# Kernel optimization log

Measured on AMD Instinct MI355X. Metric: run time of the kernel, lower is better.

## Reference

```python
import jax, jax.numpy as jnp
import numpy as np
from jax import lax

TWN_THRESHOLD_FACTOR = 0.05
BN_EPS = 1e-5


@jax.custom_vjp
def _ternary_quant(w, t):
    return (w > t).astype(w.dtype) - (w < -t).astype(w.dtype)

def _tq_fwd(w, t):
    mask = (w > t) | (w < -t)
    return _ternary_quant(w, t), mask

def _tq_bwd(mask, g):
    return (g * mask.astype(g.dtype), jnp.zeros((), g.dtype))

_ternary_quant.defvjp(_tq_fwd, _tq_bwd)


def quantize(w):
    # threshold is detached in the original (weight.detach().abs().max())
    t = TWN_THRESHOLD_FACTOR * jnp.max(jnp.abs(lax.stop_gradient(w)))
    return _ternary_quant(w, t)


def conv2d(x, w, b):
    # x: [N,C,H,W], w: [O,I,K,K], valid conv, stride 1
    y = lax.conv_general_dilated(x, w, (1, 1), 'VALID',
                                 dimension_numbers=('NCHW', 'OIHW', 'NCHW'))
    return y + b[None, :, None, None]


def maxpool2(x):
    return lax.reduce_window(x, -jnp.inf, lax.max,
                             (1, 1, 2, 2), (1, 1, 2, 2), 'VALID')


def bn2d(x, g, b):
    # training-mode batch norm over (N,H,W), biased variance
    m = jnp.mean(x, (0, 2, 3), keepdims=True)
    v = jnp.mean(jnp.square(x - m), (0, 2, 3), keepdims=True)
    return (x - m) * lax.rsqrt(v + BN_EPS) * g[None, :, None, None] + b[None, :, None, None]


def bn1d(x, g, b):
    m = jnp.mean(x, 0, keepdims=True)
    v = jnp.mean(jnp.square(x - m), 0, keepdims=True)
    return (x - m) * lax.rsqrt(v + BN_EPS) * g[None, :] + b[None, :]


def setup_inputs() -> dict:
    key = jax.random.key(0)
    ks = jax.random.split(key, 12)
    N = 4096
    inp = {
        'x': jax.random.normal(ks[0], (N, 1, 28, 28), jnp.float32),
        'w1': jax.random.normal(ks[1], (32, 1, 5, 5), jnp.float32) * 0.2,
        'b1': jnp.zeros((32,), jnp.float32),
        'g1': jnp.ones((32,), jnp.float32),
        'be1': jnp.zeros((32,), jnp.float32),
        'w2': jax.random.normal(ks[2], (64, 32, 5, 5), jnp.float32) * 0.05,
        'b2': jnp.zeros((64,), jnp.float32),
        'g2': jnp.ones((64,), jnp.float32),
        'be2': jnp.zeros((64,), jnp.float32),
        'wf1': jax.random.normal(ks[3], (512, 1024), jnp.float32) * 0.03,
        'bf1': jnp.zeros((512,), jnp.float32),
        'g3': jnp.ones((512,), jnp.float32),
        'be3': jnp.zeros((512,), jnp.float32),
        'wf2': jax.random.normal(ks[4], (10, 512), jnp.float32) * 0.04,
        'bf2': jnp.zeros((10,), jnp.float32),
    }
    return inp


def reference(x, w1, b1, g1, be1, w2, b2, g2, be2, wf1, bf1, g3, be3, wf2, bf2):
    h = jax.nn.relu(bn2d(conv2d(x, quantize(w1), b1), g1, be1))     # [N,32,24,24]
    h = maxpool2(h)                                                  # [N,32,12,12]
    h = jax.nn.relu(bn2d(conv2d(h, quantize(w2), b2), g2, be2))     # [N,64,8,8]
    h = maxpool2(h)                                                  # [N,64,4,4]
    h = h.reshape(h.shape[0], -1)                                    # [N,1024]
    h = jax.nn.relu(bn1d(h @ quantize(wf1).T + bf1, g3, be3))       # [N,512]
    return h @ quantize(wf2).T + bf2                                 # [N,10]
```

## Files before the change

kernel.cpp:

```cpp
#include <hip/hip_runtime.h>

#define TID ((int)threadIdx.x)
typedef unsigned short u16;
typedef short short8 __attribute__((ext_vector_type(8)));
typedef float f32x4 __attribute__((ext_vector_type(4)));
typedef float v2f __attribute__((ext_vector_type(2)));

__device__ __forceinline__ u16 f2b(float f) {
    unsigned int x = __float_as_uint(f);
    return (u16)((x + 0x7fffu + ((x >> 16) & 1u)) >> 16);
}
__device__ __forceinline__ float b2f(u16 u) {
    return __uint_as_float(((unsigned int)u) << 16);
}
__device__ __forceinline__ v2f fma2(float a, v2f b, v2f c) {
    v2f av = {a, a};
    return __builtin_elementwise_fma(av, b, c);
}

static constexpr size_t OFF_QW1   = 0;
static constexpr size_t OFF_QWF2  = 3200;
static constexpr size_t OFF_TMAX  = 23680;
static constexpr size_t OFF_SUM1C = 23808;
static constexpr size_t OFF_SSQ1C = 24832;
static constexpr size_t OFF_SUM2  = 25856, OFF_SSQ2 = 26112;
static constexpr size_t OFF_SUM3  = 26368, OFF_SSQ3 = 28416;
static constexpr size_t STATS_BEG = 23680, STATS_END = 30464;
static constexpr size_t OFF_QW2C  = 30720;
static constexpr size_t OFF_QWF1C = 133120;
static constexpr size_t OFF_Y1P   = 1181696;
static constexpr size_t OFF_H2P   = 38930432;
static constexpr size_t OFF_Y3    = 47319040;

__global__ __launch_bounds__(256) void absmax_k(const float* w1, const float* w2,
                                                const float* wf1, const float* wf2,
                                                unsigned int* tmaxbits) {
    int bid = blockIdx.x;
    int b, lb, nb; const float* src; long n;
    if (bid < 1)        { b = 0; src = w1;  n = 800;    lb = bid;       nb = 1;   }
    else if (bid < 9)   { b = 1; src = w2;  n = 51200;  lb = bid - 1;   nb = 8;   }
    else if (bid < 265) { b = 2; src = wf1; n = 524288; lb = bid - 9;   nb = 256; }
    else                { b = 3; src = wf2; n = 5120;   lb = bid - 265; nb = 1;   }
    float m = 0.f;
    for (long i = (long)lb * 256 + TID; i < n; i += (long)nb * 256)
        m = fmaxf(m, fabsf(src[i]));
    __shared__ float red[256];
    red[TID] = m; __syncthreads();
    for (int s = 128; s > 0; s >>= 1) {
        if (TID < s) red[TID] = fmaxf(red[TID], red[TID + s]);
        __syncthreads();
    }
    if (TID == 0) atomicMax(&tmaxbits[b], __float_as_uint(red[0]));
}

__global__ __launch_bounds__(256) void quant_all_k(const float* w1, const float* w2,
                                                   const float* wf1, const float* wf2,
                                                   float* qw1, u16* qw2c, u16* qwf1c,
                                                   float* qwf2, const unsigned int* tmax) {
    int bid = blockIdx.x;
    if (bid < 4) {
        int i = bid * 256 + TID; if (i >= 800) return;
        float t = 0.05f * __uint_as_float(tmax[0]);
        float v = w1[i];
        qw1[i] = (v > t) ? 1.f : ((v < -t) ? -1.f : 0.f);
    } else if (bid < 204) {
        int i = (bid - 4) * 256 + TID;
        float t = 0.05f * __uint_as_float(tmax[1]);
        int ic = i & 31, oc = (i >> 5) & 63, sh = i >> 11;
        float v = w2[(oc * 32 + ic) * 25 + sh];
        qw2c[i] = f2b((v > t) ? 1.f : ((v < -t) ? -1.f : 0.f));
    } else if (bid < 2252) {
        int i = (bid - 204) * 256 + TID;
        float t = 0.05f * __uint_as_float(tmax[2]);
        float v = wf1[i];
        qwf1c[i] = f2b((v > t) ? 1.f : ((v < -t) ? -1.f : 0.f));
    } else {
        int i = (bid - 2252) * 256 + TID;
        float t = 0.05f * __uint_as_float(tmax[3]);
        float v = wf2[i];
        qwf2[i] = (v > t) ? 1.f : ((v < -t) ? -1.f : 0.f);
    }
}

__global__ __launch_bounds__(256) void conv1_fused_k(const float* __restrict__ x,
                                                     const float* __restrict__ qw1,
                                                     u16* __restrict__ y1p,
                                                     float* sum1c, float* ssq1c) {
    __shared__ float wl[800];
    __shared__ float red[4][64];
    for (int i = TID; i < 800; i += 256) wl[i] = qw1[i];
    __syncthreads();
    int p = blockIdx.x * 256 + TID;
    int cg = p & 15, half = (p >> 4) & 1;
    int pr = p >> 5;
    int py = pr % 12, n = pr / 12;
    int l = TID & 63, wv = TID >> 6;
    const float* xb = x + n * 784 + (2 * py) * 28 + half * 12;
    float patch[6][16];
    #pragma unroll
    for (int r = 0; r < 6; r++) {
        const float4* rp = reinterpret_cast<const float4*>(xb + r * 28);
        #pragma unroll
        for (int qq = 0; qq < 4; qq++) {
            float4 v = rp[qq];
            patch[r][qq * 4 + 0] = v.x; patch[r][qq * 4 + 1] = v.y;
            patch[r][qq * 4 + 2] = v.z; patch[r][qq * 4 + 3] = v.w;
        }
    }
    int c0 = cg * 2;
    v2f wp[25];
    #pragma unroll
    for (int k = 0; k < 25; k++)
        wp[k] = (v2f){wl[c0 * 25 + k], wl[(c0 + 1) * 25 + k]};
    v2f A0[12], A1[12];
    #pragma unroll
    for (int ox = 0; ox < 12; ox++) { A0[ox] = (v2f){0.f, 0.f}; A1[ox] = (v2f){0.f, 0.f}; }
    #pragma unroll
    for (int ky = 0; ky < 5; ky++)
        #pragma unroll
        for (int kx = 0; kx < 5; kx++) {
            v2f w = wp[ky * 5 + kx];
            #pragma unroll
            for (int ox = 0; ox < 12; ox++) {
                A0[ox] = fma2(patch[ky][ox + kx], w, A0[ox]);
                A1[ox] = fma2(patch[ky + 1][ox + kx], w, A1[ox]);
            }
        }
    v2f sv = {0.f, 0.f}, qv = {0.f, 0.f};
    #pragma unroll
    for (int ox = 0; ox < 12; ox++) {
        sv += A0[ox] + A1[ox];
        qv = __builtin_elementwise_fma(A0[ox], A0[ox], qv);
        qv = __builtin_elementwise_fma(A1[ox], A1[ox], qv);
    }
    float st[4] = {sv.x, sv.y, qv.x, qv.y};
    u16* base = y1p + (size_t)n * 4608 + (py * 12 + half * 6) * 32 + c0;
    #pragma unroll
    for (int j = 0; j < 6; j++) {
        v2f pm = __builtin_elementwise_max(
                     __builtin_elementwise_max(A0[2 * j], A0[2 * j + 1]),
                     __builtin_elementwise_max(A1[2 * j], A1[2 * j + 1]));
        unsigned int u = (unsigned int)f2b(pm.x) | ((unsigned int)f2b(pm.y) << 16);
        *reinterpret_cast<unsigned int*>(base + j * 32) = u;
    }
    #pragma unroll
    for (int t = 0; t < 4; t++) {
        st[t] += __shfl_xor(st[t], 16);
        st[t] += __shfl_xor(st[t], 32);
    }
    if (l < 16) {
        #pragma unroll
        for (int t = 0; t < 4; t++) red[wv][l * 4 + t] = st[t];
    }
    __syncthreads();
    if (TID < 64) {
        float v = red[0][TID] + red[1][TID] + red[2][TID] + red[3][TID];
        int t = TID & 3, ch = (TID >> 2) * 2 + (t & 1);
        float* dst = (t < 2 ? sum1c : ssq1c) + (blockIdx.x & 7) * 32 + ch;
        atomicAdd(dst, v);
    }
}

__global__ __launch_bounds__(256) void conv2_k(const u16* __restrict__ y1p,
                                               const u16* __restrict__ qw2c,
                                               u16* __restrict__ h2pre,
                                               const float* sum1c, const float* ssq1c,
                                               const float* g1, const float* be1,
                                               float* sum, float* ssq) {
    __shared__ float4 hsm4[1176];
    __shared__ float scs[32], shs[32];
    char* hsraw = (char*)hsm4;
    int n0 = blockIdx.x * 8;
    int l = TID & 63, wv = TID >> 6;
    int oc0 = wv * 16;
    int lm = l & 15, lr = (l >> 3) & 1, ox = l & 7, bq = l >> 4;
    if (TID < 32) {
        float s = 0.f, q = 0.f;
        #pragma unroll
        for (int r = 0; r < 8; r++) { s += sum1c[r * 32 + TID]; q += ssq1c[r * 32 + TID]; }
        float m = s * (1.f / 2359296.f);
        float v = q * (1.f / 2359296.f) - m * m;
        float sc = g1[TID] / sqrtf(v + 1e-5f);
        scs[TID] = sc; shs[TID] = be1[TID] - m * sc;
    }
    __syncthreads();
    float scR[8], shR[8];
    {
        int b = TID & 3;
        #pragma unroll
        for (int j = 0; j < 8; j++) { scR[j] = scs[b * 8 + j]; shR[j] = shs[b * 8 + j]; }
    }
    short8 bw[25];
    #pragma unroll
    for (int sh = 0; sh < 25; sh++)
        bw[sh] = *reinterpret_cast<const short8*>(qw2c + ((size_t)sh * 64 + oc0 + lm) * 32 + bq * 8);
    int xy[5];
    #pragma unroll
    for (int kx = 0; kx < 5; kx++) {
        int xx = ox + kx;
        xy[kx] = lr * 784 + xx * 64 + (((bq + (xx >> 1)) & 3) * 16);
    }
    float sacc = 0.f, s2acc = 0.f;
    {
        const uint4* src = reinterpret_cast<const uint4*>(y1p + (size_t)n0 * 4608);
        #pragma unroll
        for (int k = 0; k < 3; k++) {
            if (k < 2 || TID < 64) {
                int i = TID + k * 256;
                int pix = i >> 2, b = i & 3;
                int y = pix / 12, xx = pix - y * 12;
                union { uint4 v; u16 u[8]; } in, out;
                in.v = src[i];
                #pragma unroll
                for (int j = 0; j < 8; j++)
                    out.u[j] = f2b(fmaxf(fmaf(b2f(in.u[j]), scR[j], shR[j]), 0.f));
                *reinterpret_cast<uint4*>(hsraw + y * 784 + xx * 64 + (((b + (xx >> 1)) & 3) * 16)) = out.v;
            }
        }
    }
    #pragma unroll 1
    for (int s = 0; s < 8; s++) {
        __syncthreads();
        if (s < 7) {
            const uint4* src = reinterpret_cast<const uint4*>(y1p + (size_t)(n0 + s + 1) * 4608);
            char* dst = hsraw + ((s + 1) & 1) * 9408;
            #pragma unroll
            for (int k = 0; k < 3; k++) {
                if (k < 2 || TID < 64) {
                    int i = TID + k * 256;
                    int pix = i >> 2, b = i & 3;
                    int y = pix / 12, xx = pix - y * 12;
                    union { uint4 v; u16 u[8]; } in, out;
                    in.v = src[i];
                    #pragma unroll
                    for (int j = 0; j < 8; j++)
                        out.u[j] = f2b(fmaxf(fmaf(b2f(in.u[j]), scR[j], shR[j]), 0.f));
                    *reinterpret_cast<uint4*>(dst + y * 784 + xx * 64 + (((b + (xx >> 1)) & 3) * 16)) = out.v;
                }
            }
        }
        const char* hb = hsraw + (s & 1) * 9408;
        f32x4 acc[4] = {{0.f,0.f,0.f,0.f},{0.f,0.f,0.f,0.f},{0.f,0.f,0.f,0.f},{0.f,0.f,0.f,0.f}};
        #pragma unroll
        for (int R = 0; R <= 10; R++) {
            short8 a[5];
            #pragma unroll
            for (int kx = 0; kx < 5; kx++)
                a[kx] = *reinterpret_cast<const short8*>(hb + xy[kx] + R * 784);
            #pragma unroll
            for (int mt = 0; mt < 4; mt++) {
                int ky = R - 2 * mt;
                if (ky < 0 || ky > 4) continue;
                #pragma unroll
                for (int kx = 0; kx < 5; kx++)
                    acc[mt] = __builtin_amdgcn_mfma_f32_16x16x32_bf16(a[kx], bw[ky * 5 + kx], acc[mt], 0, 0, 0);
            }
        }
        int n = n0 + s;
        u16* hp = h2pre + (size_t)n * 1024 + (oc0 + lm) * 16;
        #pragma unroll
        for (int mt = 0; mt < 4; mt++) {
            float v0 = acc[mt][0], v1 = acc[mt][1], v2 = acc[mt][2], v3 = acc[mt][3];
            sacc += v0 + v1 + v2 + v3;
            s2acc += v0 * v0 + v1 * v1 + v2 * v2 + v3 * v3;
            float w0 = fmaxf(v0, v1), w1 = fmaxf(v2, v3);
            float p0 = fmaxf(w0, __shfl_xor(w0, 32));
            float p1 = fmaxf(w1, __shfl_xor(w1, 32));
            if (bq < 2) {
                unsigned int u = (unsigned int)f2b(p0) | ((unsigned int)f2b(p1) << 16);
                *reinterpret_cast<unsigned int*>(hp + mt * 4 + bq * 2) = u;
            }
        }
    }
    sacc  += __shfl_xor(sacc, 16);  sacc  += __shfl_xor(sacc, 32);
    s2acc += __shfl_xor(s2acc, 16); s2acc += __shfl_xor(s2acc, 32);
    if (l < 16) { atomicAdd(&sum[oc0 + l], sacc); atomicAdd(&ssq[oc0 + l], s2acc); }
}

__global__ __launch_bounds__(256) void fc1_k(const u16* __restrict__ h2pre,
                                             const u16* __restrict__ qwf1c,
                                             const float* sum2, const float* ssq2,
                                             const float* g2, const float* be2,
                                             float* __restrict__ y3T,
                                             float* sum3, float* ssq3) {
    __shared__ float4 Asm[576], Bsm[576];
    __shared__ float sc2s[64], sh2s[64];
    u16* AsU = (u16*)Asm; u16* BsU = (u16*)Bsm;
    int m0 = blockIdx.x * 64, j0 = blockIdx.y * 64;
    int l = TID & 63, wv = TID >> 6;
    int lm = l & 15, q = l >> 4;
    int r0 = TID >> 3, c0 = TID & 7;
    if (TID < 64) {
        float m = sum2[TID] * (1.f / 262144.f);
        float v = ssq2[TID] * (1.f / 262144.f) - m * m;
        float s = g2[TID] / sqrtf(v + 1e-5f);
        sc2s[TID] = s; sh2s[TID] = be2[TID] - m * s;
    }
    __syncthreads();
    f32x4 acc[4] = {{0.f,0.f,0.f,0.f},{0.f,0.f,0.f,0.f},{0.f,0.f,0.f,0.f},{0.f,0.f,0.f,0.f}};
    #pragma unroll 1
    for (int kc = 0; kc < 16; kc++) {
        int kk = kc * 64;
        if (kc) __syncthreads();
        int oc = (kk + c0 * 8) >> 4;
        float sc = sc2s[oc], sh = sh2s[oc];
        #pragma unroll
        for (int i = 0; i < 2; i++) {
            int r = i * 32 + r0;
            union { float4 v; u16 h[8]; } in, o;
            in.v = *reinterpret_cast<const float4*>(h2pre + (size_t)(m0 + r) * 1024 + kk + c0 * 8);
            #pragma unroll
            for (int e = 0; e < 8; e++)
                o.h[e] = f2b(fmaxf(fmaf(b2f(in.h[e]), sc, sh), 0.f));
            *reinterpret_cast<float4*>(AsU + r * 72 + c0 * 8) = o.v;
            *reinterpret_cast<float4*>(BsU + r * 72 + c0 * 8) =
                *reinterpret_cast<const float4*>(qwf1c + (size_t)(j0 + r) * 1024 + kk + c0 * 8);
        }
        __syncthreads();
        #pragma unroll
        for (int half = 0; half < 2; half++) {
            short8 b = *reinterpret_cast<const short8*>(BsU + (wv * 16 + lm) * 72 + half * 32 + q * 8);
            #pragma unroll
            for (int mt = 0; mt < 4; mt++) {
                short8 a = *reinterpret_cast<const short8*>(AsU + (mt * 16 + lm) * 72 + half * 32 + q * 8);
                acc[mt] = __builtin_amdgcn_mfma_f32_16x16x32_bf16(a, b, acc[mt], 0, 0, 0);
            }
        }
    }
    float s = 0.f, s2 = 0.f;
    #pragma unroll
    for (int mt = 0; mt < 4; mt++) {
        *reinterpret_cast<f32x4*>(y3T + (size_t)(j0 + wv * 16 + lm) * 4096 + m0 + mt * 16 + q * 4) = acc[mt];
        #pragma unroll
        for (int i = 0; i < 4; i++) { float v = acc[mt][i]; s += v; s2 = fmaf(v, v, s2); }
    }
    s  += __shfl_xor(s, 16);  s  += __shfl_xor(s, 32);
    s2 += __shfl_xor(s2, 16); s2 += __shfl_xor(s2, 32);
    if (l < 16) {
        atomicAdd(&sum3[j0 + wv * 16 + l], s);
        atomicAdd(&ssq3[j0 + wv * 16 + l], s2);
    }
}

__global__ __launch_bounds__(256) void fc2_k(const float* __restrict__ y3T,
                                             const float* sum3, const float* ssq3,
                                             const float* g3, const float* be3,
                                             const float* __restrict__ qwf2,
                                             const float* bf2, float* __restrict__ out) {
    __shared__ float wlds[5120];
    __shared__ float part[15][160];
    __shared__ float sc3s[512], sh3s[512];
    for (int i = TID; i < 5120; i += 256) wlds[i] = qwf2[i];
    for (int k = TID; k < 512; k += 256) {
        float m = sum3[k] * (1.f / 4096.f);
        float v = ssq3[k] * (1.f / 4096.f) - m * m;
        float s = g3[k] / sqrtf(v + 1e-5f);
        sc3s[k] = s; sh3s[k] = be3[k] - m * s;
    }
    __syncthreads();
    int nl = TID & 15, ks = TID >> 4;
    int n = blockIdx.x * 16 + nl;
    float acc[10] = {};
    for (int k = ks * 32; k < ks * 32 + 32; k++) {
        float v = fmaxf(y3T[(size_t)k * 4096 + n] * sc3s[k] + sh3s[k], 0.f);
        #pragma unroll
        for (int o = 0; o < 10; o++) acc[o] = fmaf(v, wlds[o * 512 + k], acc[o]);
    }
    if (ks > 0) {
        #pragma unroll
        for (int o = 0; o < 10; o++) part[ks - 1][o * 16 + nl] = acc[o];
    }
    __syncthreads();
    if (ks == 0) {
        #pragma unroll
        for (int o = 0; o < 10; o++) {
            float r = acc[o] + bf2[o];
            #pragma unroll
            for (int j = 0; j < 15; j++) r += part[j][o * 16 + nl];
            out[n * 10 + o] = r;
        }
    }
}

extern "C" void kernel_launch(void* const* d_in, const int* in_sizes, int n_in,
                              void* d_out, int out_size, void* d_ws, size_t ws_size,
                              hipStream_t stream) {
    char* wsb = (char*)d_ws;
    const float* x   = (const float*)d_in[0];
    const float* w1  = (const float*)d_in[1];
    const float* g1  = (const float*)d_in[3];
    const float* be1 = (const float*)d_in[4];
    const float* w2  = (const float*)d_in[5];
    const float* g2  = (const float*)d_in[7];
    const float* be2 = (const float*)d_in[8];
    const float* wf1 = (const float*)d_in[9];
    const float* g3  = (const float*)d_in[11];
    const float* be3 = (const float*)d_in[12];
    const float* wf2 = (const float*)d_in[13];
    const float* bf2 = (const float*)d_in[14];
    float* out = (float*)d_out;

    unsigned int* tmax = (unsigned int*)(wsb + OFF_TMAX);
    float* qw1   = (float*)(wsb + OFF_QW1);
    float* qwf2  = (float*)(wsb + OFF_QWF2);
    u16*   qw2c  = (u16*)(wsb + OFF_QW2C);
    u16*   qwf1c = (u16*)(wsb + OFF_QWF1C);
    u16*   y1p   = (u16*)(wsb + OFF_Y1P);
    u16*   h2pre = (u16*)(wsb + OFF_H2P);
    float* y3    = (float*)(wsb + OFF_Y3);

    float* sum1c = (float*)(wsb + OFF_SUM1C); float* ssq1c = (float*)(wsb + OFF_SSQ1C);
    float* sum2  = (float*)(wsb + OFF_SUM2);  float* ssq2  = (float*)(wsb + OFF_SSQ2);
    float* sum3  = (float*)(wsb + OFF_SUM3);  float* ssq3  = (float*)(wsb + OFF_SSQ3);

    hipMemsetAsync(wsb + STATS_BEG, 0, STATS_END - STATS_BEG, stream);

    absmax_k<<<266, 256, 0, stream>>>(w1, w2, wf1, wf2, tmax);
    quant_all_k<<<2272, 256, 0, stream>>>(w1, w2, wf1, wf2, qw1, qw2c, qwf1c, qwf2, tmax);

    conv1_fused_k<<<6144, 256, 0, stream>>>(x, qw1, y1p, sum1c, ssq1c);
    conv2_k<<<512, 256, 0, stream>>>(y1p, qw2c, h2pre, sum1c, ssq1c, g1, be1, sum2, ssq2);
    fc1_k<<<dim3(64, 8), 256, 0, stream>>>(h2pre, qwf1c, sum2, ssq2, g2, be2, y3, sum3, ssq3);
    fc2_k<<<256, 256, 0, stream>>>(y3, sum3, ssq3, g3, be3, qwf2, bf2, out);
}
```

Before: 232.5 us.

## Fuse fc1 and fc2 into one cooperative kernel with a grid-wide sync

```diff
diff --git a/kernel.cpp b/kernel.cpp
--- a/kernel.cpp
+++ b/kernel.cpp
@@ -1,4 +1,7 @@
 #include <hip/hip_runtime.h>
+#include <hip/hip_cooperative_groups.h>
+
+namespace cg = cooperative_groups;
 
 #define TID ((int)threadIdx.x)
 typedef unsigned short u16;
@@ -30,7 +33,6 @@
 static constexpr size_t OFF_QWF1C = 133120;
 static constexpr size_t OFF_Y1P   = 1181696;
 static constexpr size_t OFF_H2P   = 38930432;
-static constexpr size_t OFF_Y3    = 47319040;
 
 __global__ __launch_bounds__(256) void absmax_k(const float* w1, const float* w2,
                                                 const float* wf1, const float* wf2,
@@ -91,7 +93,7 @@
     for (int i = TID; i < 800; i += 256) wl[i] = qw1[i];
     __syncthreads();
     int p = blockIdx.x * 256 + TID;
-    int cg = p & 15, half = (p >> 4) & 1;
+    int cg_ = p & 15, half = (p >> 4) & 1;
     int pr = p >> 5;
     int py = pr % 12, n = pr / 12;
     int l = TID & 63, wv = TID >> 6;
@@ -107,7 +109,7 @@
             patch[r][qq * 4 + 2] = v.z; patch[r][qq * 4 + 3] = v.w;
         }
     }
-    int c0 = cg * 2;
+    int c0 = cg_ * 2;
     v2f wp[25];
     #pragma unroll
     for (int k = 0; k < 25; k++)
@@ -277,16 +279,24 @@
     if (l < 16) { atomicAdd(&sum[oc0 + l], sacc); atomicAdd(&ssq[oc0 + l], s2acc); }
 }
 
-__global__ __launch_bounds__(256) void fc1_k(const u16* __restrict__ h2pre,
-                                             const u16* __restrict__ qwf1c,
-                                             const float* sum2, const float* ssq2,
-                                             const float* g2, const float* be2,
-                                             float* __restrict__ y3T,
-                                             float* sum3, float* ssq3) {
+__global__ __launch_bounds__(256) void fc12_k(const u16* __restrict__ h2pre,
+                                              const u16* __restrict__ qwf1c,
+                                              const float* sum2, const float* ssq2,
+                                              const float* g2, const float* be2,
+                                              const float* __restrict__ qwf2,
+                                              const float* g3, const float* be3,
+                                              const float* bf2,
+                                              float* sum3, float* ssq3,
+                                              float* __restrict__ out) {
     __shared__ float4 Asm[576], Bsm[576];
     __shared__ float sc2s[64], sh2s[64];
+    __shared__ u16 vls[64 * 74];
+    __shared__ float part[3][640];
+    __shared__ float wsl[640];
     u16* AsU = (u16*)Asm; u16* BsU = (u16*)Bsm;
-    int m0 = blockIdx.x * 64, j0 = blockIdx.y * 64;
+    int bid = blockIdx.x;
+    int jb = bid & 7, mb = bid >> 3;
+    int j0 = jb * 64;
     int l = TID & 63, wv = TID >> 6;
     int lm = l & 15, q = l >> 4;
     int r0 = TID >> 3, c0 = TID & 7;
@@ -296,88 +306,99 @@
         float s = g2[TID] / sqrtf(v + 1e-5f);
         sc2s[TID] = s; sh2s[TID] = be2[TID] - m * s;
     }
+    for (int i = TID; i < 640; i += 256) {
+        int jj = i / 10, o = i - jj * 10;
+        wsl[jj * 10 + o] = qwf2[o * 512 + j0 + jj];
+    }
     __syncthreads();
-    f32x4 acc[4] = {{0.f,0.f,0.f,0.f},{0.f,0.f,0.f,0.f},{0.f,0.f,0.f,0.f},{0.f,0.f,0.f,0.f}};
+    f32x4 acc[2][4] = {};
     #pragma unroll 1
-    for (int kc = 0; kc < 16; kc++) {
-        int kk = kc * 64;
-        if (kc) __syncthreads();
-        int oc = (kk + c0 * 8) >> 4;
-        float sc = sc2s[oc], sh = sh2s[oc];
-        #pragma unroll
-        for (int i = 0; i < 2; i++) {
-            int r = i * 32 + r0;
-            union { float4 v; u16 h[8]; } in, o;
-            in.v = *reinterpret_cast<const float4*>(h2pre + (size_t)(m0 + r) * 1024 + kk + c0 * 8);
-            #pragma unroll
-            for (int e = 0; e < 8; e++)
-                o.h[e] = f2b(fmaxf(fmaf(b2f(in.h[e]), sc, sh), 0.f));
-            *reinterpret_cast<float4*>(AsU + r * 72 + c0 * 8) = o.v;
-            *reinterpret_cast<float4*>(BsU + r * 72 + c0 * 8) =
-                *reinterpret_cast<const float4*>(qwf1c + (size_t)(j0 + r) * 1024 + kk + c0 * 8);
-        }
-        __syncthreads();
-        #pragma unroll
-        for (int half = 0; half < 2; half++) {
-            short8 b = *reinterpret_cast<const short8*>(BsU + (wv * 16 + lm) * 72 + half * 32 + q * 8);
-            #pragma unroll
-            for (int mt = 0; mt < 4; mt++) {
-                short8 a = *reinterpret_cast<const short8*>(AsU + (mt * 16 + lm) * 72 + half * 32 + q * 8);
-                acc[mt] = __builtin_amdgcn_mfma_f32_16x16x32_bf16(a, b, acc[mt], 0, 0, 0);
+    for (int t = 0; t < 2; t++) {
+        int m0 = (mb * 2 + t) * 64;
+        #pragma unroll 1
+        for (int kc = 0; kc < 16; kc++) {
+            int kk = kc * 64;
+            if (kc | t) __syncthreads();
+            int oc = (kk + c0 * 8) >> 4;
+            float sc = sc2s[oc], sh = sh2s[oc];
+            #pragma unroll
+            for (int i = 0; i < 2; i++) {
+                int r = i * 32 + r0;
+                union { float4 v; u16 h[8]; } in, o;
+                in.v = *reinterpret_cast<const float4*>(h2pre + (size_t)(m0 + r) * 1024 + kk + c0 * 8);
+                #pragma unroll
+                for (int e = 0; e < 8; e++)
+                    o.h[e] = f2b(fmaxf(fmaf(b2f(in.h[e]), sc, sh), 0.f));
+                *reinterpret_cast<float4*>(AsU + r * 72 + c0 * 8) = o.v;
+                *reinterpret_cast<float4*>(BsU + r * 72 + c0 * 8) =
+                    *reinterpret_cast<const float4*>(qwf1c + (size_t)(j0 + r) * 1024 + kk + c0 * 8);
+            }
+            __syncthreads();
+            #pragma unroll
+            for (int half = 0; half < 2; half++) {
+                short8 b = *reinterpret_cast<const short8*>(BsU + (wv * 16 + lm) * 72 + half * 32 + q * 8);
+                #pragma unroll
+                for (int mt = 0; mt < 4; mt++) {
+                    short8 a = *reinterpret_cast<const short8*>(AsU + (mt * 16 + lm) * 72 + half * 32 + q * 8);
+                    acc[t][mt] = __builtin_amdgcn_mfma_f32_16x16x32_bf16(a, b, acc[t][mt], 0, 0, 0);
+                }
             }
         }
     }
     float s = 0.f, s2 = 0.f;
     #pragma unroll
-    for (int mt = 0; mt < 4; mt++) {
-        *reinterpret_cast<f32x4*>(y3T + (size_t)(j0 + wv * 16 + lm) * 4096 + m0 + mt * 16 + q * 4) = acc[mt];
-        #pragma unroll
-        for (int i = 0; i < 4; i++) { float v = acc[mt][i]; s += v; s2 = fmaf(v, v, s2); }
-    }
+    for (int t = 0; t < 2; t++)
+        #pragma unroll
+        for (int mt = 0; mt < 4; mt++)
+            #pragma unroll
+            for (int i = 0; i < 4; i++) { float v = acc[t][mt][i]; s += v; s2 = fmaf(v, v, s2); }
     s  += __shfl_xor(s, 16);  s  += __shfl_xor(s, 32);
     s2 += __shfl_xor(s2, 16); s2 += __shfl_xor(s2, 32);
     if (l < 16) {
         atomicAdd(&sum3[j0 + wv * 16 + l], s);
         atomicAdd(&ssq3[j0 + wv * 16 + l], s2);
     }
-}
-
-__global__ __launch_bounds__(256) void fc2_k(const float* __restrict__ y3T,
-                                             const float* sum3, const float* ssq3,
-                                             const float* g3, const float* be3,
-                                             const float* __restrict__ qwf2,
-                                             const float* bf2, float* __restrict__ out) {
-    __shared__ float wlds[5120];
-    __shared__ float part[15][160];
-    __shared__ float sc3s[512], sh3s[512];
-    for (int i = TID; i < 5120; i += 256) wlds[i] = qwf2[i];
-    for (int k = TID; k < 512; k += 256) {
-        float m = sum3[k] * (1.f / 4096.f);
-        float v = ssq3[k] * (1.f / 4096.f) - m * m;
-        float s = g3[k] / sqrtf(v + 1e-5f);
-        sc3s[k] = s; sh3s[k] = be3[k] - m * s;
-    }
-    __syncthreads();
-    int nl = TID & 15, ks = TID >> 4;
-    int n = blockIdx.x * 16 + nl;
-    float acc[10] = {};
-    for (int k = ks * 32; k < ks * 32 + 32; k++) {
-        float v = fmaxf(y3T[(size_t)k * 4096 + n] * sc3s[k] + sh3s[k], 0.f);
-        #pragma unroll
-        for (int o = 0; o < 10; o++) acc[o] = fmaf(v, wlds[o * 512 + k], acc[o]);
-    }
-    if (ks > 0) {
-        #pragma unroll
-        for (int o = 0; o < 10; o++) part[ks - 1][o * 16 + nl] = acc[o];
-    }
-    __syncthreads();
-    if (ks == 0) {
-        #pragma unroll
-        for (int o = 0; o < 10; o++) {
-            float r = acc[o] + bf2[o];
-            #pragma unroll
-            for (int j = 0; j < 15; j++) r += part[j][o * 16 + nl];
-            out[n * 10 + o] = r;
+    __threadfence();
+    cg::this_grid().sync();
+    int j = j0 + wv * 16 + lm;
+    float m3 = sum3[j] * (1.f / 4096.f);
+    float v3 = ssq3[j] * (1.f / 4096.f) - m3 * m3;
+    float sc3 = g3[j] / sqrtf(v3 + 1e-5f);
+    float sh3 = be3[j] - m3 * sc3;
+    int jl = wv * 16 + lm;
+    int ml = TID & 63, grp = TID >> 6;
+    #pragma unroll 1
+    for (int t = 0; t < 2; t++) {
+        int m0 = (mb * 2 + t) * 64;
+        __syncthreads();
+        #pragma unroll
+        for (int mt = 0; mt < 4; mt++)
+            #pragma unroll
+            for (int i = 0; i < 4; i++) {
+                int mrow = mt * 16 + q * 4 + i;
+                vls[mrow * 74 + jl] = f2b(fmaxf(fmaf(acc[t][mt][i], sc3, sh3), 0.f));
+            }
+        __syncthreads();
+        float o10[10] = {};
+        #pragma unroll
+        for (int jj = 0; jj < 16; jj++) {
+            float vj = b2f(vls[ml * 74 + grp * 16 + jj]);
+            #pragma unroll
+            for (int o = 0; o < 10; o++)
+                o10[o] = fmaf(vj, wsl[(grp * 16 + jj) * 10 + o], o10[o]);
+        }
+        if (grp > 0) {
+            #pragma unroll
+            for (int o = 0; o < 10; o++) part[grp - 1][o * 64 + ml] = o10[o];
+        }
+        __syncthreads();
+        if (grp == 0) {
+            #pragma unroll
+            for (int o = 0; o < 10; o++) {
+                float r = o10[o] + part[0][o * 64 + ml] + part[1][o * 64 + ml]
+                          + part[2][o * 64 + ml] + (jb == 0 ? bf2[o] : 0.f);
+                atomicAdd(&out[(m0 + ml) * 10 + o], r);
+            }
         }
     }
 }
@@ -407,19 +428,22 @@
     u16*   qwf1c = (u16*)(wsb + OFF_QWF1C);
     u16*   y1p   = (u16*)(wsb + OFF_Y1P);
     u16*   h2pre = (u16*)(wsb + OFF_H2P);
-    float* y3    = (float*)(wsb + OFF_Y3);
 
     float* sum1c = (float*)(wsb + OFF_SUM1C); float* ssq1c = (float*)(wsb + OFF_SSQ1C);
     float* sum2  = (float*)(wsb + OFF_SUM2);  float* ssq2  = (float*)(wsb + OFF_SSQ2);
     float* sum3  = (float*)(wsb + OFF_SUM3);  float* ssq3  = (float*)(wsb + OFF_SSQ3);
 
     hipMemsetAsync(wsb + STATS_BEG, 0, STATS_END - STATS_BEG, stream);
+    hipMemsetAsync(out, 0, 4096 * 10 * sizeof(float), stream);
 
     absmax_k<<<266, 256, 0, stream>>>(w1, w2, wf1, wf2, tmax);
     quant_all_k<<<2272, 256, 0, stream>>>(w1, w2, wf1, wf2, qw1, qw2c, qwf1c, qwf2, tmax);
 
     conv1_fused_k<<<6144, 256, 0, stream>>>(x, qw1, y1p, sum1c, ssq1c);
     conv2_k<<<512, 256, 0, stream>>>(y1p, qw2c, h2pre, sum1c, ssq1c, g1, be1, sum2, ssq2);
-    fc1_k<<<dim3(64, 8), 256, 0, stream>>>(h2pre, qwf1c, sum2, ssq2, g2, be2, y3, sum3, ssq3);
-    fc2_k<<<256, 256, 0, stream>>>(y3, sum3, ssq3, g3, be3, qwf2, bf2, out);
-}
+
+    void* args[] = {(void*)&h2pre, (void*)&qwf1c, (void*)&sum2, (void*)&ssq2,
+                    (void*)&g2, (void*)&be2, (void*)&qwf2, (void*)&g3, (void*)&be3,
+                    (void*)&bf2, (void*)&sum3, (void*)&ssq3, (void*)&out};
+    hipLaunchCooperativeKernel((void*)fc12_k, dim3(256), dim3(256), args, 0, stream);
+}
```

Result: slower. 342.6 us (+47.4%).

## Rewrite conv1 as bf16 MFMA implicit GEMM with LDS-staged input tiles

Applied to the files above, without the earlier changes.

```diff
diff --git a/kernel.cpp b/kernel.cpp
--- a/kernel.cpp
+++ b/kernel.cpp
@@ -4,7 +4,6 @@
 typedef unsigned short u16;
 typedef short short8 __attribute__((ext_vector_type(8)));
 typedef float f32x4 __attribute__((ext_vector_type(4)));
-typedef float v2f __attribute__((ext_vector_type(2)));
 
 __device__ __forceinline__ u16 f2b(float f) {
     unsigned int x = __float_as_uint(f);
@@ -12,10 +11,6 @@
 }
 __device__ __forceinline__ float b2f(u16 u) {
     return __uint_as_float(((unsigned int)u) << 16);
-}
-__device__ __forceinline__ v2f fma2(float a, v2f b, v2f c) {
-    v2f av = {a, a};
-    return __builtin_elementwise_fma(av, b, c);
 }
 
 static constexpr size_t OFF_QW1   = 0;
@@ -86,78 +81,111 @@
                                                      const float* __restrict__ qw1,
                                                      u16* __restrict__ y1p,
                                                      float* sum1c, float* ssq1c) {
-    __shared__ float wl[800];
-    __shared__ float red[4][64];
-    for (int i = TID; i < 800; i += 256) wl[i] = qw1[i];
-    __syncthreads();
-    int p = blockIdx.x * 256 + TID;
-    int cg = p & 15, half = (p >> 4) & 1;
-    int pr = p >> 5;
-    int py = pr % 12, n = pr / 12;
-    int l = TID & 63, wv = TID >> 6;
-    const float* xb = x + n * 784 + (2 * py) * 28 + half * 12;
-    float patch[6][16];
-    #pragma unroll
-    for (int r = 0; r < 6; r++) {
-        const float4* rp = reinterpret_cast<const float4*>(xb + r * 28);
-        #pragma unroll
-        for (int qq = 0; qq < 4; qq++) {
-            float4 v = rp[qq];
-            patch[r][qq * 4 + 0] = v.x; patch[r][qq * 4 + 1] = v.y;
-            patch[r][qq * 4 + 2] = v.z; patch[r][qq * 4 + 3] = v.w;
-        }
-    }
-    int c0 = cg * 2;
-    v2f wp[25];
-    #pragma unroll
-    for (int k = 0; k < 25; k++)
-        wp[k] = (v2f){wl[c0 * 25 + k], wl[(c0 + 1) * 25 + k]};
-    v2f A0[12], A1[12];
-    #pragma unroll
-    for (int ox = 0; ox < 12; ox++) { A0[ox] = (v2f){0.f, 0.f}; A1[ox] = (v2f){0.f, 0.f}; }
-    #pragma unroll
-    for (int ky = 0; ky < 5; ky++)
-        #pragma unroll
-        for (int kx = 0; kx < 5; kx++) {
-            v2f w = wp[ky * 5 + kx];
-            #pragma unroll
-            for (int ox = 0; ox < 12; ox++) {
-                A0[ox] = fma2(patch[ky][ox + kx], w, A0[ox]);
-                A1[ox] = fma2(patch[ky + 1][ox + kx], w, A1[ox]);
-            }
-        }
-    v2f sv = {0.f, 0.f}, qv = {0.f, 0.f};
-    #pragma unroll
-    for (int ox = 0; ox < 12; ox++) {
-        sv += A0[ox] + A1[ox];
-        qv = __builtin_elementwise_fma(A0[ox], A0[ox], qv);
-        qv = __builtin_elementwise_fma(A1[ox], A1[ox], qv);
-    }
-    float st[4] = {sv.x, sv.y, qv.x, qv.y};
-    u16* base = y1p + (size_t)n * 4608 + (py * 12 + half * 6) * 32 + c0;
-    #pragma unroll
-    for (int j = 0; j < 6; j++) {
-        v2f pm = __builtin_elementwise_max(
-                     __builtin_elementwise_max(A0[2 * j], A0[2 * j + 1]),
-                     __builtin_elementwise_max(A1[2 * j], A1[2 * j + 1]));
-        unsigned int u = (unsigned int)f2b(pm.x) | ((unsigned int)f2b(pm.y) << 16);
-        *reinterpret_cast<unsigned int*>(base + j * 32) = u;
-    }
-    #pragma unroll
-    for (int t = 0; t < 4; t++) {
-        st[t] += __shfl_xor(st[t], 16);
-        st[t] += __shfl_xor(st[t], 32);
-    }
+    __shared__ __align__(16) u16 xs[16 * 1096];
+    int gid = blockIdx.x;
+    int sg = gid >> 2, ph = (gid >> 1) & 1, pch = gid & 1;
+    int l = TID & 63, w = TID >> 6;
+    int lm = l & 15, q = l >> 4;
+
+    #pragma unroll
+    for (int i = 0; i < 9; i++) {
+        int idx = TID + i * 256;
+        if (idx < 2192) reinterpret_cast<uint4*>(xs)[idx] = make_uint4(0, 0, 0, 0);
+    }
+
+    short8 B1[2], B2[2];
+    #pragma unroll
+    for (int c = 0; c < 2; c++) {
+        union { short8 s; u16 h[8]; } b1, b2;
+        int ch = c * 16 + lm;
+        #pragma unroll
+        for (int j = 0; j < 8; j++) {
+            float v1 = 0.f, v2 = 0.f;
+            if (j < 5) {
+                v1 = qw1[ch * 25 + q * 5 + j];
+                v2 = qw1[ch * 25 + 20 + j];
+            }
+            b1.h[j] = f2b(v1);
+            b2.h[j] = (q == 0) ? f2b(v2) : (u16)0;
+        }
+        B1[c] = b1.s; B2[c] = b2.s;
+    }
+    __syncthreads();
+
+    #pragma unroll
+    for (int k = 0; k < 7; k++) {
+        int i = TID + k * 256;
+        int smp = i / 112, rem = i % 112;
+        int row = rem / 7, c4 = (rem % 7) * 4;
+        float4 v = *reinterpret_cast<const float4*>(
+            x + (size_t)(sg * 16 + smp) * 784 + (12 * ph + row) * 28 + c4);
+        u16 h[4] = {f2b(v.x), f2b(v.y), f2b(v.z), f2b(v.w)};
+        union { uint2 u; u16 hh[4]; } pk;
+        pk.hh[0] = h[0]; pk.hh[1] = h[1]; pk.hh[2] = h[2]; pk.hh[3] = h[3];
+        *reinterpret_cast<uint2*>(xs + smp * 1096 + row * 32 + c4) = pk.u;
+        u16* b1p = xs + smp * 1096 + 548 + row * 32;
+        #pragma unroll
+        for (int e = 0; e < 4; e++) {
+            int c = c4 + e;
+            if (c >= 1) b1p[c - 1] = h[e];
+        }
+    }
+    __syncthreads();
+
+    float s0 = 0.f, s1 = 0.f, q0 = 0.f, q1 = 0.f;
+    int laneoff = lm * 1096;
+    #pragma unroll 1
+    for (int e = 0; e < 9; e++) {
+        int pp = w * 9 + e;
+        int prl = pp / 6, pcl = pp - prl * 6;
+        f32x4 pm0 = {-3.0e38f, -3.0e38f, -3.0e38f, -3.0e38f};
+        f32x4 pm1 = pm0;
+        #pragma unroll
+        for (int dyx = 0; dyx < 4; dyx++) {
+            int dy = dyx >> 1, dx = dyx & 1;
+            int oyl = 2 * prl + dy;
+            int ox = 2 * (pch * 6 + pcl) + dx;
+            int r = ox & 1, cb = ox - r;
+            const u16* p1 = xs + laneoff + r * 548 + (oyl + q) * 32 + cb;
+            const u16* p2 = xs + laneoff + r * 548 + (oyl + 4) * 32 + cb;
+            union { short8 s; unsigned int u[4]; } a1, a2;
+            #pragma unroll
+            for (int t = 0; t < 4; t++) {
+                a1.u[t] = *reinterpret_cast<const unsigned int*>(p1 + 2 * t);
+                a2.u[t] = *reinterpret_cast<const unsigned int*>(p2 + 2 * t);
+            }
+            f32x4 d0 = {0.f, 0.f, 0.f, 0.f};
+            d0 = __builtin_amdgcn_mfma_f32_16x16x32_bf16(a1.s, B1[0], d0, 0, 0, 0);
+            d0 = __builtin_amdgcn_mfma_f32_16x16x32_bf16(a2.s, B2[0], d0, 0, 0, 0);
+            f32x4 d1 = {0.f, 0.f, 0.f, 0.f};
+            d1 = __builtin_amdgcn_mfma_f32_16x16x32_bf16(a1.s, B1[1], d1, 0, 0, 0);
+            d1 = __builtin_amdgcn_mfma_f32_16x16x32_bf16(a2.s, B2[1], d1, 0, 0, 0);
+            #pragma unroll
+            for (int i = 0; i < 4; i++) {
+                float v = d0[i]; s0 += v; q0 = fmaf(v, v, q0);
+                float u = d1[i]; s1 += u; q1 = fmaf(u, u, q1);
+            }
+            pm0 = __builtin_elementwise_max(pm0, d0);
+            pm1 = __builtin_elementwise_max(pm1, d1);
+        }
+        int ppg = (ph * 6 + prl) * 12 + (pch * 6 + pcl);
+        #pragma unroll
+        for (int i = 0; i < 4; i++) {
+            size_t nb = (size_t)(sg * 16 + 4 * q + i) * 4608 + ppg * 32;
+            y1p[nb + lm]      = f2b(pm0[i]);
+            y1p[nb + 16 + lm] = f2b(pm1[i]);
+        }
+    }
+    s0 += __shfl_xor(s0, 16); s0 += __shfl_xor(s0, 32);
+    s1 += __shfl_xor(s1, 16); s1 += __shfl_xor(s1, 32);
+    q0 += __shfl_xor(q0, 16); q0 += __shfl_xor(q0, 32);
+    q1 += __shfl_xor(q1, 16); q1 += __shfl_xor(q1, 32);
     if (l < 16) {
-        #pragma unroll
-        for (int t = 0; t < 4; t++) red[wv][l * 4 + t] = st[t];
-    }
-    __syncthreads();
-    if (TID < 64) {
-        float v = red[0][TID] + red[1][TID] + red[2][TID] + red[3][TID];
-        int t = TID & 3, ch = (TID >> 2) * 2 + (t & 1);
-        float* dst = (t < 2 ? sum1c : ssq1c) + (blockIdx.x & 7) * 32 + ch;
-        atomicAdd(dst, v);
+        int slot = (blockIdx.x & 7) * 32;
+        atomicAdd(&sum1c[slot + l], s0);
+        atomicAdd(&sum1c[slot + 16 + l], s1);
+        atomicAdd(&ssq1c[slot + l], q0);
+        atomicAdd(&ssq1c[slot + 16 + l], q1);
     }
 }
 
@@ -418,7 +446,7 @@
     absmax_k<<<266, 256, 0, stream>>>(w1, w2, wf1, wf2, tmax);
     quant_all_k<<<2272, 256, 0, stream>>>(w1, w2, wf1, wf2, qw1, qw2c, qwf1c, qwf2, tmax);
 
-    conv1_fused_k<<<6144, 256, 0, stream>>>(x, qw1, y1p, sum1c, ssq1c);
+    conv1_fused_k<<<1024, 256, 0, stream>>>(x, qw1, y1p, sum1c, ssq1c);
     conv2_k<<<512, 256, 0, stream>>>(y1p, qw2c, h2pre, sum1c, ssq1c, g1, be1, sum2, ssq2);
     fc1_k<<<dim3(64, 8), 256, 0, stream>>>(h2pre, qwf1c, sum2, ssq2, g2, be2, y3, sum3, ssq3);
     fc2_k<<<256, 256, 0, stream>>>(y3, sum3, ssq3, g3, be3, qwf2, bf2, out);
```

After: 211.3 us. 1.1x faster.
